# Optimization experiments

Hardware: AMD Instinct MI355X
Metric: run time of the kernel (lower is better)

The kernel has to match this reference:

```python
import jax, jax.numpy as jnp
import numpy as np

# Static graph/problem sizes
N = 20000      # num_node
E = 320000     # num_edge (already includes inverse relations)
B = 4          # number of query rows (batch)
K = 32         # candidate tails per row
D = 32         # input_dim == hidden_dim
R = 20         # num_relation
DR = 2 * R     # double_relation (with inverses)
T = 10         # time_steps
TAU = 4.0
VTH = 2.0
DECAY_RATIO = 0.95
LINEAR_SCALE = 1.0
ALPHA = 4.0    # surrogate.Sigmoid(alpha=4.0)


@jax.custom_vjp
def spike_fn(x):
    # Heaviside forward, sigmoid surrogate gradient (surrogate.Sigmoid(alpha=4))
    return (x >= 0.0).astype(x.dtype)

def _spike_fwd(x):
    return spike_fn(x), x

def _spike_bwd(x, g):
    sg = jax.nn.sigmoid(ALPHA * x)
    return (g * ALPHA * sg * (1.0 - sg),)

spike_fn.defvjp(_spike_fwd, _spike_bwd)


def setup_inputs() -> dict:
    key = jax.random.key(0)
    ks = jax.random.split(key, 16)
    return {
        "edge_src": jax.random.randint(ks[0], (E,), 0, N),
        "edge_dst": jax.random.randint(ks[1], (E,), 0, N),
        "edge_type": jax.random.randint(ks[2], (E,), 0, DR),
        "h_index": jax.random.randint(ks[3], (B,), 0, N),
        "t_index": jax.random.randint(ks[4], (B, K), 0, N),
        "r_index": jax.random.randint(ks[5], (B,), 0, R),
        "query_emb": jax.random.normal(ks[6], (DR, D), jnp.float32) * 0.1,
        "relw_W": jax.random.normal(ks[7], (D, DR * D), jnp.float32) * 0.1,
        "relw_b": jnp.zeros((DR * D,), jnp.float32),
        "lin_W": jax.random.normal(ks[8], (D, D), jnp.float32) * 0.1,
        "lin_b": jnp.zeros((D,), jnp.float32),
        "mlp_W1": jax.random.normal(ks[9], (2 * D, 2 * D), jnp.float32) * 0.1,
        "mlp_b1": jnp.zeros((2 * D,), jnp.float32),
        "mlp_W2": jax.random.normal(ks[10], (1, 2 * D), jnp.float32) * 0.1,
        "mlp_b2": jnp.zeros((1,), jnp.float32),
    }


def reference(edge_src, edge_dst, edge_type, h_index, t_index, r_index,
              query_emb, relw_W, relw_b, lin_W, lin_b,
              mlp_W1, mlp_b1, mlp_W2, mlp_b2):
    # --- query / boundary (snn_forward prologue) ---
    query = query_emb[r_index]                      # (B, D)
    q_scaled = query * (VTH / 2) + VTH / 2          # boundary_query scaling
    boundary = jnp.zeros((N, B, D), query.dtype).at[h_index, jnp.arange(B)].add(q_scaled)

    # dependent relation weights: Linear(input_dim -> DR*input_dim) applied to query
    w_rel = (query @ relw_W + relw_b).reshape(B, DR, D)    # (B, DR, D)
    w_edge = jnp.transpose(w_rel[:, edge_type], (1, 0, 2)) # (E, B, D)

    # --- initial LIF state ---
    s0 = spike_fn(boundary - VTH)
    v0 = boundary * (1.0 - s0)
    c0 = jnp.zeros_like(boundary)
    decay = jnp.exp(jnp.float32(-1.0 / TAU))

    def step(carry, _):
        s, v, c = carry
        # relational message passing: gather source spikes, relation-weight, scatter-sum
        msg = s[edge_src] * w_edge                             # (E, B, D)
        agg = jax.ops.segment_sum(msg, edge_dst, num_segments=N)
        x = (agg @ lin_W.T + lin_b) * LINEAR_SCALE             # (N, B, D)
        # alpha-synapse LIF dynamics
        c = c * decay + x
        v = v * decay + c
        s_new = spike_fn(v - VTH)
        v = v * (1.0 - s_new)                                  # soft reset
        return (s_new, v, c), s_new

    _, s_seq = jax.lax.scan(step, (s0, v0, c0), None, length=T - 1)
    spikes = jnp.concatenate([s0[None], s_seq], axis=0)        # (T, N, B, D)

    # final temporal kernel: logspace decay, normalized by geometric sum
    r = DECAY_RATIO
    n_scale = (1.0 - r ** T) / (1.0 - r)
    kernel = (r ** jnp.arange(T, dtype=jnp.float32)) / n_scale # (T,)
    enc = jnp.einsum('tnbd,t->nbd', spikes, kernel)            # (N, B, D)

    node_query = jnp.broadcast_to(query[None], (N, B, D))
    out = jnp.concatenate([enc, node_query], axis=-1)          # (N, B, 2D)

    # gather tail candidates and score with 2-layer MLP
    feat = jnp.transpose(out, (1, 0, 2))[jnp.arange(B)[:, None], t_index]  # (B, K, 2D)
    h = jax.nn.relu(feat @ mlp_W1.T + mlp_b1)
    score = (h @ mlp_W2.T + mlp_b2)[..., 0]                    # (B, K)
    return score
```

## Files before the change

kernel.cpp:

```cpp
#include <hip/hip_runtime.h>

#define NN 20000
#define EE 320000
#define BB 4
#define KK 32
#define DD 32
#define DRR 40
#define TT 10

#define NPB 32
#define NGRP 8
#define NPG 4
#define MTHR 256
#define NBLK_MEGA 625
#define MAXDEG 128

static constexpr float VTH = 2.0f;
static constexpr float DECAY = 0.7788007831f;
static constexpr float K0 = 0.12460655f;

__global__ __launch_bounds__(256) void prep_all_kernel(
    const int* __restrict__ h_index, const int* __restrict__ r_index,
    const float* __restrict__ query_emb, const float* __restrict__ relw_W,
    const float* __restrict__ relw_b, const float* __restrict__ lin_b,
    float* __restrict__ w_rel, float* __restrict__ query,
    unsigned* __restrict__ sb0, int* __restrict__ cnt, int* __restrict__ bars,
    int* __restrict__ flag)
{
    __shared__ int sf;
    const int tid = threadIdx.x;
    const int t = blockIdx.x * 256 + tid;

    if (blockIdx.x == 0 && tid == 0) sf = 0;

    if (t < 5120) {
        int b = t / (DRR * DD);
        int o = t % (DRR * DD);
        int typ = o >> 5, d = o & 31;
        int ri = r_index[b];
        float acc = relw_b[o];
        for (int i = 0; i < DD; ++i)
            acc += query_emb[ri * DD + i] * relw_W[i * (DRR * DD) + o];
        w_rel[typ * (DD * BB) + d * BB + b] = acc;
    } else if (t < 25120) {
        cnt[t - 5120] = 0;
    } else if (t < 45120) {
        int n = t - 25120;
        uint4 wv = make_uint4(0u, 0u, 0u, 0u);
        unsigned* wp = &wv.x;
        #pragma unroll
        for (int b = 0; b < BB; ++b) {
            if (n == h_index[b]) {
                int ri = r_index[b];
                unsigned w = 0;
                for (int d = 0; d < DD; ++d)
                    w |= (query_emb[ri * DD + d] >= 1.0f ? 1u : 0u) << d;
                wp[b] = w;
            }
        }
        *(uint4*)(sb0 + n * BB) = wv;
    } else if (t < 45248) {
        int i = t - 45120;
        query[i] = query_emb[r_index[i >> 5] * DD + (i & 31)];
    } else if (t < 45264) {
        bars[t - 45248] = 0;
    }

    if (blockIdx.x == 0) {
        __syncthreads();
        if (tid < 128) {
            int b = tid >> 5, d = tid & 31;
            int pred = (query_emb[r_index[b] * DD + d] >= 1.0f);
            if (tid < DD && lin_b[tid] != 0.0f) pred = 1;
            if (pred) atomicOr(&sf, 1);
        }
        __syncthreads();
        if (tid == 0) *flag = sf;
    }
}

__device__ __forceinline__ void grid_barrier(int* bars, int idx)
{
    __syncthreads();
    if (threadIdx.x == 0) {
        __threadfence();
        atomicAdd(&bars[idx], 1);
        while (atomicAdd(&bars[idx], 0) < NBLK_MEGA)
            __builtin_amdgcn_s_sleep(16);
        __threadfence();
    }
    __syncthreads();
}

__global__ __launch_bounds__(MTHR, 3) void mega_kernel(
    const int* __restrict__ flag,
    const int* __restrict__ edge_src, const int* __restrict__ edge_dst,
    const int* __restrict__ edge_type,
    int* __restrict__ cnt, unsigned* __restrict__ col2,
    unsigned* __restrict__ sb0, unsigned* __restrict__ sb1,
    const float* __restrict__ w_rel, const float* __restrict__ lin_W,
    const float* __restrict__ lin_b, float* __restrict__ v, float* __restrict__ c,
    const int* __restrict__ h_index, const float* __restrict__ query,
    const int* __restrict__ t_index, float* __restrict__ enc, int* __restrict__ bars)
{
    if (*flag == 0) return;

    __shared__ unsigned stg_u[NGRP][DD];
    __shared__ uint4 stg_sb[NGRP][DD];
    __shared__ float lds_agg[NGRP][BB][DD];

    const int tid = threadIdx.x, bid = blockIdx.x;
    const int d = tid & 31;
    const int g = tid >> 5;
    const int l = tid & 63;
    const int n0 = bid * NPB + g * NPG;
    const float bias = lin_b[d];

    for (int e = bid * MTHR + tid; e < EE; e += NBLK_MEGA * MTHR) {
        int dn = edge_dst[e];
        int pos = atomicAdd(&cnt[dn], 1);
        if (pos < MAXDEG)
            col2[dn * MAXDEG + pos] = (unsigned)edge_src[e] | ((unsigned)edge_type[e] << 16);
    }
    grid_barrier(bars, 0);

    unsigned* cur = sb0;
    unsigned* nxt = sb1;
    float kt = K0;

    for (int t = 1; t < TT; ++t) {
        const int first = (t == 1);

        if (bid == 0) {
            for (int i = tid; i < BB * KK * DD; i += MTHR) {
                int row = i >> 5, dd = i & 31;
                int b = row >> 5;
                int node = t_index[row];
                float bit = (float)((cur[node * BB + b] >> dd) & 1);
                float val = kt * bit;
                enc[i] = first ? val : (enc[i] + val);
            }
        }

        for (int k = 0; k < NPG; ++k) {
            const int n = n0 + k;
            const int e0 = n * MAXDEG;
            const int e1 = e0 + min(cnt[n], MAXDEG);

            float4 vv, cc;
            if (first) {
                float vt[BB];
                #pragma unroll
                for (int b = 0; b < BB; ++b) {
                    float bd = (n == h_index[b]) ? (query[b * DD + d] + 1.0f) : 0.0f;
                    vt[b] = (bd >= VTH) ? 0.0f : bd;
                }
                vv = make_float4(vt[0], vt[1], vt[2], vt[3]);
                cc = make_float4(0.f, 0.f, 0.f, 0.f);
            } else {
                vv = *(const float4*)(v + n * (DD * BB) + d * 4);
                cc = *(const float4*)(c + n * (DD * BB) + d * 4);
            }

            float agg0 = 0.f, agg1 = 0.f, agg2 = 0.f, agg3 = 0.f;
            for (int base = e0; base < e1; base += DD) {
                int eidx = base + d;
                unsigned u = 0;
                uint4 sv = make_uint4(0u, 0u, 0u, 0u);
                if (eidx < e1) {
                    u = col2[eidx];
                    sv = *(const uint4*)(cur + (u & 0xFFFFu) * BB);
                }
                stg_u[g][d] = u;
                stg_sb[g][d] = sv;
                int ne = min(DD, e1 - base);
                for (int j = 0; j < ne; ++j) {
                    uint4 sj = stg_sb[g][j];
                    if ((sj.x | sj.y | sj.z | sj.w) == 0u) continue;
                    unsigned uj = stg_u[g][j];
                    float4 wv = __ldg((const float4*)w_rel + (uj >> 16) * DD + d);
                    agg0 += ((sj.x >> d) & 1u) ? wv.x : 0.0f;
                    agg1 += ((sj.y >> d) & 1u) ? wv.y : 0.0f;
                    agg2 += ((sj.z >> d) & 1u) ? wv.z : 0.0f;
                    agg3 += ((sj.w >> d) & 1u) ? wv.w : 0.0f;
                }
            }

            float xs[BB];
            bool anyact = __any((agg0 != 0.f) | (agg1 != 0.f) | (agg2 != 0.f) | (agg3 != 0.f));
            if (anyact) {
                lds_agg[g][0][d] = agg0;
                lds_agg[g][1][d] = agg1;
                lds_agg[g][2][d] = agg2;
                lds_agg[g][3][d] = agg3;
                float4 Wr[8];
                #pragma unroll
                for (int q = 0; q < 8; ++q)
                    Wr[q] = *(const float4*)(lin_W + d * DD + q * 4);
                #pragma unroll
                for (int b = 0; b < BB; ++b) {
                    float x = bias;
                    #pragma unroll
                    for (int q = 0; q < 8; ++q) {
                        float4 a4 = *(const float4*)&lds_agg[g][b][q * 4];
                        x += a4.x * Wr[q].x + a4.y * Wr[q].y + a4.z * Wr[q].z + a4.w * Wr[q].w;
                    }
                    xs[b] = x;
                }
            } else {
                #pragma unroll
                for (int b = 0; b < BB; ++b) xs[b] = bias;
            }

            float cn, vn;
            cn = cc.x * DECAY + xs[0]; vn = vv.x * DECAY + cn; int s0 = (vn >= VTH); cc.x = cn; vv.x = s0 ? 0.0f : vn;
            cn = cc.y * DECAY + xs[1]; vn = vv.y * DECAY + cn; int s1 = (vn >= VTH); cc.y = cn; vv.y = s1 ? 0.0f : vn;
            cn = cc.z * DECAY + xs[2]; vn = vv.z * DECAY + cn; int s2 = (vn >= VTH); cc.z = cn; vv.z = s2 ? 0.0f : vn;
            cn = cc.w * DECAY + xs[3]; vn = vv.w * DECAY + cn; int s3 = (vn >= VTH); cc.w = cn; vv.w = s3 ? 0.0f : vn;

            *(float4*)(v + n * (DD * BB) + d * 4) = vv;
            *(float4*)(c + n * (DD * BB) + d * 4) = cc;

            unsigned long long m0 = __ballot(s0);
            unsigned long long m1 = __ballot(s1);
            unsigned long long m2 = __ballot(s2);
            unsigned long long m3 = __ballot(s3);
            if (l == 0) {
                nxt[n * BB + 0] = (unsigned)m0;
                nxt[n * BB + 1] = (unsigned)m1;
                nxt[n * BB + 2] = (unsigned)m2;
                nxt[n * BB + 3] = (unsigned)m3;
            } else if (l == 32) {
                nxt[n * BB + 0] = (unsigned)(m0 >> 32);
                nxt[n * BB + 1] = (unsigned)(m1 >> 32);
                nxt[n * BB + 2] = (unsigned)(m2 >> 32);
                nxt[n * BB + 3] = (unsigned)(m3 >> 32);
            }
        }

        if (t < TT - 1) grid_barrier(bars, t);
        unsigned* tmp = cur; cur = nxt; nxt = tmp;
        kt *= 0.95f;
    }
}

__global__ __launch_bounds__(64) void final_fix_kernel(
    const int* __restrict__ flag,
    const int* __restrict__ t_index, const unsigned* __restrict__ sb_last,
    const float* __restrict__ enc, const float* __restrict__ query,
    const float* __restrict__ W1, const float* __restrict__ b1,
    const float* __restrict__ W2, const float* __restrict__ b2,
    float* __restrict__ out, float klast)
{
    __shared__ float w1t[64 * 65];
    __shared__ float feat[2 * DD];
    int tid = threadIdx.x;
    int row = blockIdx.x, b = row >> 5;
    int active = *flag;
    for (int idx = tid; idx < 64 * 64; idx += 64) {
        int j = idx >> 6, i = idx & 63;
        w1t[i * 65 + j] = W1[idx];
    }
    if (tid < DD) {
        float e = 0.0f;
        if (active) {
            unsigned w = sb_last[t_index[row] * BB + b];
            e = enc[row * DD + tid] + klast * (float)((w >> tid) & 1u);
        }
        feat[tid] = e;
        feat[DD + tid] = query[b * DD + tid];
    }
    __syncthreads();
    float h = b1[tid];
    #pragma unroll
    for (int i = 0; i < 2 * DD; ++i)
        h += feat[i] * w1t[i * 65 + tid];
    float part = W2[tid] * fmaxf(h, 0.0f);
    #pragma unroll
    for (int off = 32; off >= 1; off >>= 1)
        part += __shfl_xor(part, off, 64);
    if (tid == 0) out[row] = part + b2[0];
}

extern "C" void kernel_launch(void* const* d_in, const int* in_sizes, int n_in,
                              void* d_out, int out_size, void* d_ws, size_t ws_size,
                              hipStream_t stream)
{
    const int*   edge_src  = (const int*)d_in[0];
    const int*   edge_dst  = (const int*)d_in[1];
    const int*   edge_type = (const int*)d_in[2];
    const int*   h_index   = (const int*)d_in[3];
    const int*   t_index   = (const int*)d_in[4];
    const int*   r_index   = (const int*)d_in[5];
    const float* query_emb = (const float*)d_in[6];
    const float* relw_W    = (const float*)d_in[7];
    const float* relw_b    = (const float*)d_in[8];
    const float* lin_W     = (const float*)d_in[9];
    const float* lin_b     = (const float*)d_in[10];
    const float* mlp_W1    = (const float*)d_in[11];
    const float* mlp_b1    = (const float*)d_in[12];
    const float* mlp_W2    = (const float*)d_in[13];
    const float* mlp_b2    = (const float*)d_in[14];
    float* out = (float*)d_out;

    unsigned* sb0     = (unsigned*)d_ws;
    unsigned* sb1     = sb0 + NN * BB;
    float*    w_rel   = (float*)(sb1 + NN * BB);
    float*    query   = w_rel + BB * DRR * DD;
    float*    enc     = query + BB * DD;
    int*      cnt     = (int*)(enc + BB * KK * DD);
    int*      flagp   = cnt + NN;
    int*      bars    = flagp + 16;
    unsigned* col2    = (unsigned*)(bars + 16);
    float*    v       = (float*)(col2 + NN * MAXDEG);
    float*    c       = v + NN * BB * DD;

    float r = 0.95f;
    float ns = (1.0f - powf(r, (float)TT)) / (1.0f - r);
    float klast = powf(r, (float)(TT - 1)) / ns;

    prep_all_kernel<<<177, 256, 0, stream>>>(
        h_index, r_index, query_emb, relw_W, relw_b, lin_b,
        w_rel, query, sb0, cnt, bars, flagp);
    mega_kernel<<<NBLK_MEGA, MTHR, 0, stream>>>(
        flagp, edge_src, edge_dst, edge_type, cnt, col2, sb0, sb1,
        w_rel, lin_W, lin_b, v, c, h_index, query, t_index, enc, bars);
    final_fix_kernel<<<BB * KK, 64, 0, stream>>>(
        flagp, t_index, sb1, enc, query, mlp_W1, mlp_b1, mlp_W2, mlp_b2,
        out, klast);
}
```

Baseline: 14.23 us.

## Fold prep and final MLP kernels into the persistent mega kernel

Shrinks the prep kernel to a single block that only writes the query, the activity flag and the barrier counters. The w_rel projection, degree-count zeroing and initial spike bitmask now run inside the mega kernel, behind an extra grid barrier, and only when the flag says spiking can happen. The tail MLP scoring moves into the first 32 blocks of the mega kernel, run after a final grid barrier when the flag is set. This removes one launch and the redundant prep work on the inactive path, but adds grid barriers and extra shared memory to the persistent kernel.

```diff
diff --git a/kernel.cpp b/kernel.cpp
--- a/kernel.cpp
+++ b/kernel.cpp
@@ -19,64 +19,26 @@
 static constexpr float DECAY = 0.7788007831f;
 static constexpr float K0 = 0.12460655f;
 
-__global__ __launch_bounds__(256) void prep_all_kernel(
-    const int* __restrict__ h_index, const int* __restrict__ r_index,
-    const float* __restrict__ query_emb, const float* __restrict__ relw_W,
-    const float* __restrict__ relw_b, const float* __restrict__ lin_b,
-    float* __restrict__ w_rel, float* __restrict__ query,
-    unsigned* __restrict__ sb0, int* __restrict__ cnt, int* __restrict__ bars,
-    int* __restrict__ flag)
+__global__ __launch_bounds__(256) void init_kernel(
+    const int* __restrict__ r_index, const float* __restrict__ query_emb,
+    const float* __restrict__ lin_b, float* __restrict__ query,
+    int* __restrict__ bars, int* __restrict__ flag)
 {
     __shared__ int sf;
-    const int tid = threadIdx.x;
-    const int t = blockIdx.x * 256 + tid;
-
-    if (blockIdx.x == 0 && tid == 0) sf = 0;
-
-    if (t < 5120) {
-        int b = t / (DRR * DD);
-        int o = t % (DRR * DD);
-        int typ = o >> 5, d = o & 31;
-        int ri = r_index[b];
-        float acc = relw_b[o];
-        for (int i = 0; i < DD; ++i)
-            acc += query_emb[ri * DD + i] * relw_W[i * (DRR * DD) + o];
-        w_rel[typ * (DD * BB) + d * BB + b] = acc;
-    } else if (t < 25120) {
-        cnt[t - 5120] = 0;
-    } else if (t < 45120) {
-        int n = t - 25120;
-        uint4 wv = make_uint4(0u, 0u, 0u, 0u);
-        unsigned* wp = &wv.x;
-        #pragma unroll
-        for (int b = 0; b < BB; ++b) {
-            if (n == h_index[b]) {
-                int ri = r_index[b];
-                unsigned w = 0;
-                for (int d = 0; d < DD; ++d)
-                    w |= (query_emb[ri * DD + d] >= 1.0f ? 1u : 0u) << d;
-                wp[b] = w;
-            }
-        }
-        *(uint4*)(sb0 + n * BB) = wv;
-    } else if (t < 45248) {
-        int i = t - 45120;
-        query[i] = query_emb[r_index[i >> 5] * DD + (i & 31)];
-    } else if (t < 45264) {
-        bars[t - 45248] = 0;
+    int tid = threadIdx.x;
+    if (tid == 0) sf = 0;
+    if (tid < 16) bars[tid] = 0;
+    __syncthreads();
+    if (tid < 128) {
+        int b = tid >> 5, d = tid & 31;
+        float q = query_emb[r_index[b] * DD + d];
+        query[tid] = q;
+        int pred = (q >= 1.0f);
+        if (tid < DD && lin_b[tid] != 0.0f) pred = 1;
+        if (pred) atomicOr(&sf, 1);
     }
-
-    if (blockIdx.x == 0) {
-        __syncthreads();
-        if (tid < 128) {
-            int b = tid >> 5, d = tid & 31;
-            int pred = (query_emb[r_index[b] * DD + d] >= 1.0f);
-            if (tid < DD && lin_b[tid] != 0.0f) pred = 1;
-            if (pred) atomicOr(&sf, 1);
-        }
-        __syncthreads();
-        if (tid == 0) *flag = sf;
-    }
+    __syncthreads();
+    if (tid == 0) *flag = sf;
 }
 
 __device__ __forceinline__ void grid_barrier(int* bars, int idx)
@@ -98,188 +60,222 @@
     const int* __restrict__ edge_type,
     int* __restrict__ cnt, unsigned* __restrict__ col2,
     unsigned* __restrict__ sb0, unsigned* __restrict__ sb1,
-    const float* __restrict__ w_rel, const float* __restrict__ lin_W,
+    const float* __restrict__ relw_W, const float* __restrict__ relw_b,
+    float* __restrict__ w_rel, const float* __restrict__ lin_W,
     const float* __restrict__ lin_b, float* __restrict__ v, float* __restrict__ c,
     const int* __restrict__ h_index, const float* __restrict__ query,
-    const int* __restrict__ t_index, float* __restrict__ enc, int* __restrict__ bars)
+    const int* __restrict__ t_index, float* __restrict__ enc,
+    const float* __restrict__ W1, const float* __restrict__ b1,
+    const float* __restrict__ W2, const float* __restrict__ b2,
+    float* __restrict__ out, int* __restrict__ bars, float klast)
 {
-    if (*flag == 0) return;
-
     __shared__ unsigned stg_u[NGRP][DD];
     __shared__ uint4 stg_sb[NGRP][DD];
     __shared__ float lds_agg[NGRP][BB][DD];
+    __shared__ float w1t[64 * 65];
+    __shared__ float feat[4][64];
 
     const int tid = threadIdx.x, bid = blockIdx.x;
-    const int d = tid & 31;
-    const int g = tid >> 5;
-    const int l = tid & 63;
-    const int n0 = bid * NPB + g * NPG;
-    const float bias = lin_b[d];
-
-    for (int e = bid * MTHR + tid; e < EE; e += NBLK_MEGA * MTHR) {
-        int dn = edge_dst[e];
-        int pos = atomicAdd(&cnt[dn], 1);
-        if (pos < MAXDEG)
-            col2[dn * MAXDEG + pos] = (unsigned)edge_src[e] | ((unsigned)edge_type[e] << 16);
+    const int active = *flag;
+    unsigned* sb_last = sb1;
+
+    if (active) {
+        const int d = tid & 31;
+        const int g = tid >> 5;
+        const int l = tid & 63;
+        const int n0 = bid * NPB + g * NPG;
+        const float bias = lin_b[d];
+
+        const int gt = bid * MTHR + tid;
+        if (gt < 5120) {
+            int b = gt / (DRR * DD);
+            int o = gt % (DRR * DD);
+            int typ = o >> 5, dd = o & 31;
+            float acc = relw_b[o];
+            for (int i = 0; i < DD; ++i)
+                acc += query[b * DD + i] * relw_W[i * (DRR * DD) + o];
+            w_rel[typ * (DD * BB) + dd * BB + b] = acc;
+        } else if (gt < 25120) {
+            cnt[gt - 5120] = 0;
+        } else if (gt < 45120) {
+            int n = gt - 25120;
+            uint4 wv = make_uint4(0u, 0u, 0u, 0u);
+            unsigned* wp = &wv.x;
+            #pragma unroll
+            for (int b = 0; b < BB; ++b) {
+                if (n == h_index[b]) {
+                    unsigned w = 0;
+                    for (int dd = 0; dd < DD; ++dd)
+                        w |= (query[b * DD + dd] >= 1.0f ? 1u : 0u) << dd;
+                    wp[b] = w;
+                }
+            }
+            *(uint4*)(sb0 + n * BB) = wv;
+        }
+        grid_barrier(bars, 0);
+
+        for (int e = bid * MTHR + tid; e < EE; e += NBLK_MEGA * MTHR) {
+            int dn = edge_dst[e];
+            int pos = atomicAdd(&cnt[dn], 1);
+            if (pos < MAXDEG)
+                col2[dn * MAXDEG + pos] =
+                    (unsigned)edge_src[e] | ((unsigned)edge_type[e] << 16);
+        }
+        grid_barrier(bars, 1);
+
+        unsigned* cur = sb0;
+        unsigned* nxt = sb1;
+        float kt = K0;
+
+        for (int t = 1; t < TT; ++t) {
+            const int first = (t == 1);
+
+            if (bid == 0) {
+                for (int i = tid; i < BB * KK * DD; i += MTHR) {
+                    int row = i >> 5, dd = i & 31;
+                    int b = row >> 5;
+                    int node = t_index[row];
+                    float bit = (float)((cur[node * BB + b] >> dd) & 1);
+                    float val = kt * bit;
+                    enc[i] = first ? val : (enc[i] + val);
+                }
+            }
+
+            for (int k = 0; k < NPG; ++k) {
+                const int n = n0 + k;
+                const int e0 = n * MAXDEG;
+                const int e1 = e0 + min(cnt[n], MAXDEG);
+
+                float4 vv, cc;
+                if (first) {
+                    float vt[BB];
+                    #pragma unroll
+                    for (int b = 0; b < BB; ++b) {
+                        float bd = (n == h_index[b]) ? (query[b * DD + d] + 1.0f) : 0.0f;
+                        vt[b] = (bd >= VTH) ? 0.0f : bd;
+                    }
+                    vv = make_float4(vt[0], vt[1], vt[2], vt[3]);
+                    cc = make_float4(0.f, 0.f, 0.f, 0.f);
+                } else {
+                    vv = *(const float4*)(v + n * (DD * BB) + d * 4);
+                    cc = *(const float4*)(c + n * (DD * BB) + d * 4);
+                }
+
+                float agg0 = 0.f, agg1 = 0.f, agg2 = 0.f, agg3 = 0.f;
+                for (int base = e0; base < e1; base += DD) {
+                    int eidx = base + d;
+                    unsigned u = 0;
+                    uint4 sv = make_uint4(0u, 0u, 0u, 0u);
+                    if (eidx < e1) {
+                        u = col2[eidx];
+                        sv = *(const uint4*)(cur + (u & 0xFFFFu) * BB);
+                    }
+                    stg_u[g][d] = u;
+                    stg_sb[g][d] = sv;
+                    int ne = min(DD, e1 - base);
+                    for (int j = 0; j < ne; ++j) {
+                        uint4 sj = stg_sb[g][j];
+                        if ((sj.x | sj.y | sj.z | sj.w) == 0u) continue;
+                        unsigned uj = stg_u[g][j];
+                        float4 wv = __ldg((const float4*)w_rel + (uj >> 16) * DD + d);
+                        agg0 += ((sj.x >> d) & 1u) ? wv.x : 0.0f;
+                        agg1 += ((sj.y >> d) & 1u) ? wv.y : 0.0f;
+                        agg2 += ((sj.z >> d) & 1u) ? wv.z : 0.0f;
+                        agg3 += ((sj.w >> d) & 1u) ? wv.w : 0.0f;
+                    }
+                }
+
+                float xs[BB];
+                bool anyact = __any((agg0 != 0.f) | (agg1 != 0.f) |
+                                    (agg2 != 0.f) | (agg3 != 0.f));
+                if (anyact) {
+                    lds_agg[g][0][d] = agg0;
+                    lds_agg[g][1][d] = agg1;
+                    lds_agg[g][2][d] = agg2;
+                    lds_agg[g][3][d] = agg3;
+                    float4 Wr[8];
+                    #pragma unroll
+                    for (int q = 0; q < 8; ++q)
+                        Wr[q] = *(const float4*)(lin_W + d * DD + q * 4);
+                    #pragma unroll
+                    for (int b = 0; b < BB; ++b) {
+                        float x = bias;
+                        #pragma unroll
+                        for (int q = 0; q < 8; ++q) {
+                            float4 a4 = *(const float4*)&lds_agg[g][b][q * 4];
+                            x += a4.x * Wr[q].x + a4.y * Wr[q].y +
+                                 a4.z * Wr[q].z + a4.w * Wr[q].w;
+                        }
+                        xs[b] = x;
+                    }
+                } else {
+                    #pragma unroll
+                    for (int b = 0; b < BB; ++b) xs[b] = bias;
+                }
+
+                float cn, vn;
+                cn = cc.x * DECAY + xs[0]; vn = vv.x * DECAY + cn; int s0 = (vn >= VTH); cc.x = cn; vv.x = s0 ? 0.0f : vn;
+                cn = cc.y * DECAY + xs[1]; vn = vv.y * DECAY + cn; int s1 = (vn >= VTH); cc.y = cn; vv.y = s1 ? 0.0f : vn;
+                cn = cc.z * DECAY + xs[2]; vn = vv.z * DECAY + cn; int s2 = (vn >= VTH); cc.z = cn; vv.z = s2 ? 0.0f : vn;
+                cn = cc.w * DECAY + xs[3]; vn = vv.w * DECAY + cn; int s3 = (vn >= VTH); cc.w = cn; vv.w = s3 ? 0.0f : vn;
+
+                *(float4*)(v + n * (DD * BB) + d * 4) = vv;
+                *(float4*)(c + n * (DD * BB) + d * 4) = cc;
+
+                unsigned long long m0 = __ballot(s0);
+                unsigned long long m1 = __ballot(s1);
+                unsigned long long m2 = __ballot(s2);
+                unsigned long long m3 = __ballot(s3);
+                if (l == 0) {
+                    nxt[n * BB + 0] = (unsigned)m0;
+                    nxt[n * BB + 1] = (unsigned)m1;
+                    nxt[n * BB + 2] = (unsigned)m2;
+                    nxt[n * BB + 3] = (unsigned)m3;
+                } else if (l == 32) {
+                    nxt[n * BB + 0] = (unsigned)(m0 >> 32);
+                    nxt[n * BB + 1] = (unsigned)(m1 >> 32);
+                    nxt[n * BB + 2] = (unsigned)(m2 >> 32);
+                    nxt[n * BB + 3] = (unsigned)(m3 >> 32);
+                }
+            }
+
+            if (t < TT - 1) grid_barrier(bars, 1 + t);
+            unsigned* tmp = cur; cur = nxt; nxt = tmp;
+            kt *= 0.95f;
+        }
+        sb_last = cur;
+        grid_barrier(bars, 10);
     }
-    grid_barrier(bars, 0);
-
-    unsigned* cur = sb0;
-    unsigned* nxt = sb1;
-    float kt = K0;
-
-    for (int t = 1; t < TT; ++t) {
-        const int first = (t == 1);
-
-        if (bid == 0) {
-            for (int i = tid; i < BB * KK * DD; i += MTHR) {
-                int row = i >> 5, dd = i & 31;
-                int b = row >> 5;
-                int node = t_index[row];
-                float bit = (float)((cur[node * BB + b] >> dd) & 1);
-                float val = kt * bit;
-                enc[i] = first ? val : (enc[i] + val);
+
+    if (bid < 32) {
+        for (int idx = tid; idx < 64 * 64; idx += MTHR) {
+            int j = idx >> 6, i = idx & 63;
+            w1t[i * 65 + j] = W1[idx];
+        }
+        int r2 = tid >> 6, j = tid & 63;
+        int row = bid * 4 + r2, b = row >> 5;
+        float f;
+        if (j < DD) {
+            f = 0.0f;
+            if (active) {
+                unsigned w = sb_last[t_index[row] * BB + b];
+                f = enc[row * DD + j] + klast * (float)((w >> j) & 1u);
             }
-        }
-
-        for (int k = 0; k < NPG; ++k) {
-            const int n = n0 + k;
-            const int e0 = n * MAXDEG;
-            const int e1 = e0 + min(cnt[n], MAXDEG);
-
-            float4 vv, cc;
-            if (first) {
-                float vt[BB];
-                #pragma unroll
-                for (int b = 0; b < BB; ++b) {
-                    float bd = (n == h_index[b]) ? (query[b * DD + d] + 1.0f) : 0.0f;
-                    vt[b] = (bd >= VTH) ? 0.0f : bd;
-                }
-                vv = make_float4(vt[0], vt[1], vt[2], vt[3]);
-                cc = make_float4(0.f, 0.f, 0.f, 0.f);
-            } else {
-                vv = *(const float4*)(v + n * (DD * BB) + d * 4);
-                cc = *(const float4*)(c + n * (DD * BB) + d * 4);
-            }
-
-            float agg0 = 0.f, agg1 = 0.f, agg2 = 0.f, agg3 = 0.f;
-            for (int base = e0; base < e1; base += DD) {
-                int eidx = base + d;
-                unsigned u = 0;
-                uint4 sv = make_uint4(0u, 0u, 0u, 0u);
-                if (eidx < e1) {
-                    u = col2[eidx];
-                    sv = *(const uint4*)(cur + (u & 0xFFFFu) * BB);
-                }
-                stg_u[g][d] = u;
-                stg_sb[g][d] = sv;
-                int ne = min(DD, e1 - base);
-                for (int j = 0; j < ne; ++j) {
-                    uint4 sj = stg_sb[g][j];
-                    if ((sj.x | sj.y | sj.z | sj.w) == 0u) continue;
-                    unsigned uj = stg_u[g][j];
-                    float4 wv = __ldg((const float4*)w_rel + (uj >> 16) * DD + d);
-                    agg0 += ((sj.x >> d) & 1u) ? wv.x : 0.0f;
-                    agg1 += ((sj.y >> d) & 1u) ? wv.y : 0.0f;
-                    agg2 += ((sj.z >> d) & 1u) ? wv.z : 0.0f;
-                    agg3 += ((sj.w >> d) & 1u) ? wv.w : 0.0f;
-                }
-            }
-
-            float xs[BB];
-            bool anyact = __any((agg0 != 0.f) | (agg1 != 0.f) | (agg2 != 0.f) | (agg3 != 0.f));
-            if (anyact) {
-                lds_agg[g][0][d] = agg0;
-                lds_agg[g][1][d] = agg1;
-                lds_agg[g][2][d] = agg2;
-                lds_agg[g][3][d] = agg3;
-                float4 Wr[8];
-                #pragma unroll
-                for (int q = 0; q < 8; ++q)
-                    Wr[q] = *(const float4*)(lin_W + d * DD + q * 4);
-                #pragma unroll
-                for (int b = 0; b < BB; ++b) {
-                    float x = bias;
-                    #pragma unroll
-                    for (int q = 0; q < 8; ++q) {
-                        float4 a4 = *(const float4*)&lds_agg[g][b][q * 4];
-                        x += a4.x * Wr[q].x + a4.y * Wr[q].y + a4.z * Wr[q].z + a4.w * Wr[q].w;
-                    }
-                    xs[b] = x;
-                }
-            } else {
-                #pragma unroll
-                for (int b = 0; b < BB; ++b) xs[b] = bias;
-            }
-
-            float cn, vn;
-            cn = cc.x * DECAY + xs[0]; vn = vv.x * DECAY + cn; int s0 = (vn >= VTH); cc.x = cn; vv.x = s0 ? 0.0f : vn;
-            cn = cc.y * DECAY + xs[1]; vn = vv.y * DECAY + cn; int s1 = (vn >= VTH); cc.y = cn; vv.y = s1 ? 0.0f : vn;
-            cn = cc.z * DECAY + xs[2]; vn = vv.z * DECAY + cn; int s2 = (vn >= VTH); cc.z = cn; vv.z = s2 ? 0.0f : vn;
-            cn = cc.w * DECAY + xs[3]; vn = vv.w * DECAY + cn; int s3 = (vn >= VTH); cc.w = cn; vv.w = s3 ? 0.0f : vn;
-
-            *(float4*)(v + n * (DD * BB) + d * 4) = vv;
-            *(float4*)(c + n * (DD * BB) + d * 4) = cc;
-
-            unsigned long long m0 = __ballot(s0);
-            unsigned long long m1 = __ballot(s1);
-            unsigned long long m2 = __ballot(s2);
-            unsigned long long m3 = __ballot(s3);
-            if (l == 0) {
-                nxt[n * BB + 0] = (unsigned)m0;
-                nxt[n * BB + 1] = (unsigned)m1;
-                nxt[n * BB + 2] = (unsigned)m2;
-                nxt[n * BB + 3] = (unsigned)m3;
-            } else if (l == 32) {
-                nxt[n * BB + 0] = (unsigned)(m0 >> 32);
-                nxt[n * BB + 1] = (unsigned)(m1 >> 32);
-                nxt[n * BB + 2] = (unsigned)(m2 >> 32);
-                nxt[n * BB + 3] = (unsigned)(m3 >> 32);
-            }
-        }
-
-        if (t < TT - 1) grid_barrier(bars, t);
-        unsigned* tmp = cur; cur = nxt; nxt = tmp;
-        kt *= 0.95f;
+        } else {
+            f = query[b * DD + (j - DD)];
+        }
+        feat[r2][j] = f;
+        __syncthreads();
+        float h = b1[j];
+        #pragma unroll
+        for (int i = 0; i < 2 * DD; ++i)
+            h += feat[r2][i] * w1t[i * 65 + j];
+        float part = W2[j] * fmaxf(h, 0.0f);
+        #pragma unroll
+        for (int off = 32; off >= 1; off >>= 1)
+            part += __shfl_xor(part, off, 64);
+        if (j == 0) out[row] = part + b2[0];
     }
-}
-
-__global__ __launch_bounds__(64) void final_fix_kernel(
-    const int* __restrict__ flag,
-    const int* __restrict__ t_index, const unsigned* __restrict__ sb_last,
-    const float* __restrict__ enc, const float* __restrict__ query,
-    const float* __restrict__ W1, const float* __restrict__ b1,
-    const float* __restrict__ W2, const float* __restrict__ b2,
-    float* __restrict__ out, float klast)
-{
-    __shared__ float w1t[64 * 65];
-    __shared__ float feat[2 * DD];
-    int tid = threadIdx.x;
-    int row = blockIdx.x, b = row >> 5;
-    int active = *flag;
-    for (int idx = tid; idx < 64 * 64; idx += 64) {
-        int j = idx >> 6, i = idx & 63;
-        w1t[i * 65 + j] = W1[idx];
-    }
-    if (tid < DD) {
-        float e = 0.0f;
-        if (active) {
-            unsigned w = sb_last[t_index[row] * BB + b];
-            e = enc[row * DD + tid] + klast * (float)((w >> tid) & 1u);
-        }
-        feat[tid] = e;
-        feat[DD + tid] = query[b * DD + tid];
-    }
-    __syncthreads();
-    float h = b1[tid];
-    #pragma unroll
-    for (int i = 0; i < 2 * DD; ++i)
-        h += feat[i] * w1t[i * 65 + tid];
-    float part = W2[tid] * fmaxf(h, 0.0f);
-    #pragma unroll
-    for (int off = 32; off >= 1; off >>= 1)
-        part += __shfl_xor(part, off, 64);
-    if (tid == 0) out[row] = part + b2[0];
 }
 
 extern "C" void kernel_launch(void* const* d_in, const int* in_sizes, int n_in,
@@ -319,13 +315,9 @@
     float ns = (1.0f - powf(r, (float)TT)) / (1.0f - r);
     float klast = powf(r, (float)(TT - 1)) / ns;
 
-    prep_all_kernel<<<177, 256, 0, stream>>>(
-        h_index, r_index, query_emb, relw_W, relw_b, lin_b,
-        w_rel, query, sb0, cnt, bars, flagp);
+    init_kernel<<<1, 256, 0, stream>>>(r_index, query_emb, lin_b, query, bars, flagp);
     mega_kernel<<<NBLK_MEGA, MTHR, 0, stream>>>(
         flagp, edge_src, edge_dst, edge_type, cnt, col2, sb0, sb1,
-        w_rel, lin_W, lin_b, v, c, h_index, query, t_index, enc, bars);
-    final_fix_kernel<<<BB * KK, 64, 0, stream>>>(
-        flagp, t_index, sb1, enc, query, mlp_W1, mlp_b1, mlp_W2, mlp_b2,
-        out, klast);
+        relw_W, relw_b, w_rel, lin_W, lin_b, v, c, h_index, query, t_index, enc,
+        mlp_W1, mlp_b1, mlp_W2, mlp_b2, out, bars, klast);
 }
```

Measured after the change: 13.36 us. 1.07x faster.
